# Kernel optimization log

Measured on AMD Instinct MI355X. Metric: run time of the kernel, lower is better.

Reference implementation:

```python
import jax, jax.numpy as jnp
import numpy as np

N_HEAD = 4
N_FEAT = 256
D_K = N_FEAT // N_HEAD
MAX_SEQ_LEN = 500
LN_EPS = 1e-6


def setup_inputs() -> dict:
    key = jax.random.key(0)
    ks = jax.random.split(key, 12)
    B, L, F = 64, 500, N_FEAT
    s = lambda fan_in: 1.0 / np.sqrt(fan_in)
    return {
        "q": jax.random.normal(ks[0], (B, L, F), jnp.float32),
        "k": jax.random.normal(ks[1], (B, L, F), jnp.float32),
        "v": jax.random.normal(ks[2], (B, L, F), jnp.float32),
        # weights stored as [in, out] (torch Linear transposed)
        "w_qs": jax.random.normal(ks[3], (F, F), jnp.float32) * s(F),
        "w_vs": jax.random.normal(ks[4], (F, F), jnp.float32) * s(F),
        "w1": jax.random.normal(ks[5], (D_K, D_K), jnp.float32) * s(D_K),
        "b1": jax.random.normal(ks[6], (D_K,), jnp.float32) * s(D_K),
        "w2": jax.random.normal(ks[7], (D_K, MAX_SEQ_LEN), jnp.float32) * s(D_K),
        "b2": jax.random.normal(ks[8], (MAX_SEQ_LEN,), jnp.float32) * s(D_K),
        "fc_w": jax.random.normal(ks[9], (F, F), jnp.float32) * s(F),
        "ln_g": jnp.ones((F,), jnp.float32),
        "ln_b": jnp.zeros((F,), jnp.float32),
    }


def reference(q, k, v, w_qs, w_vs, w1, b1, w2, b2, fc_w, ln_g, ln_b):
    B, L, F = q.shape
    H, dk = N_HEAD, D_K
    residual = q
    # head projections -> [B, H, L, dk]
    qh = (q @ w_qs).reshape(B, L, H, dk).transpose(0, 2, 1, 3)
    vh = (v @ w_vs).reshape(B, L, H, dk).transpose(0, 2, 1, 3)
    # dense synthesizer: relu(q W1 + b1) W2 + b2, slice to len_q
    weight = jax.nn.relu(qh @ w1 + b1)
    attn = (weight @ w2 + b2)[..., :L]            # [B, H, L, L]
    attn = jax.nn.softmax(attn, axis=-1)
    out = attn @ vh                                # [B, H, L, dk]
    out = out.transpose(0, 2, 1, 3).reshape(B, L, F)
    out = out @ fc_w + residual
    # LayerNorm(eps=1e-6)
    mu = jnp.mean(out, axis=-1, keepdims=True)
    var = jnp.var(out, axis=-1, keepdims=True)
    out = (out - mu) * jax.lax.rsqrt(var + LN_EPS) * ln_g + ln_b
    return out
```

## Files before the change

### kernel.cpp

```cpp
#include <hip/hip_runtime.h>
#include <math.h>

#define B_   64
#define L_   500
#define F_   256
#define H_   4
#define DK   64

typedef unsigned short u16;
typedef unsigned int   u32;
typedef __attribute__((ext_vector_type(8))) short short8;
typedef __attribute__((ext_vector_type(4))) float f32x4;

static __device__ __forceinline__ u16 f2bf(float f) {
    u32 u = __float_as_uint(f);
    u32 r = (u + 0x7FFFu + ((u >> 16) & 1u)) >> 16;
    return (u16)r;
}

typedef __attribute__((address_space(3))) u32 lds32;
typedef const __attribute__((address_space(1))) u32 gbl32;
static __device__ __forceinline__ void gload_lds16(const u16* g, u16* l) {
    __builtin_amdgcn_global_load_lds((gbl32*)g, (lds32*)l, 16, 0, 0);
}

__global__ __launch_bounds__(256) void prep_kernel(
    const float* __restrict__ wq, const float* __restrict__ wv,
    const float* __restrict__ fcw, const float* __restrict__ w1,
    const float* __restrict__ w2, const float* __restrict__ b2,
    u16* __restrict__ wqT, u16* __restrict__ wvT, u16* __restrict__ fcwT,
    u16* __restrict__ w1T, u16* __restrict__ w2sw,
    u16* __restrict__ qh_bf, u16* __restrict__ vhT, float* __restrict__ b2p)
{
    int t = blockIdx.x * 256 + threadIdx.x;
    int stride = gridDim.x * 256;
    for (int i = t; i < 256 * 256; i += stride) {
        int n = i >> 8, k = i & 255;
        wqT[i]  = f2bf(wq[k * 256 + n]);
        wvT[i]  = f2bf(wv[k * 256 + n]);
        fcwT[i] = f2bf(fcw[k * 256 + n]);
    }
    for (int i = t; i < 64 * 64; i += stride) {
        int n = i >> 6, k = i & 63;
        w1T[i] = f2bf(w1[k * 64 + n]);
    }
    for (int i = t; i < 512 * 64; i += stride) {
        int cc  = i >> 12;
        int row = (i >> 6) & 63;
        int kc  = i & 63;
        int n   = cc * 64 + row;
        int kl  = kc ^ ((row & 7) << 3);
        w2sw[i] = f2bf(n < 500 ? w2[kl * 500 + n] : 0.f);
    }
    for (int i = t; i < 512; i += stride)
        b2p[i] = (i < 500) ? b2[i] : -1e30f;
    for (int i = t; i < 3072; i += stride)
        qh_bf[8192000 + i] = 0;
    for (int i = t; i < 196608; i += stride) {
        int bh = i / 768;
        int r  = i - bh * 768;
        int d  = r / 12;
        int kk = 52 + (r - d * 12);
        vhT[((size_t)((bh * 8 + 7) * 64 + d)) * 64 + (kk ^ ((d & 7) << 3))] = 0;
    }
}

__global__ __launch_bounds__(512) void proj_kernel(
    const float* __restrict__ q, const float* __restrict__ v,
    const u16* __restrict__ wqT, const u16* __restrict__ wvT,
    u16* __restrict__ qh_bf, u16* __restrict__ vhT)
{
    const int which = blockIdx.y;
    const float* __restrict__ x = which ? v : q;
    const u16*   __restrict__ wT = which ? wvT : wqT;

    __shared__ u16 Xs[64][72];
    __shared__ u16 Ws[256][72];

    const int tid  = threadIdx.x;
    const int wvid = tid >> 6, ln = tid & 63;
    const int n16  = ln & 15, quad = ln >> 4;
    const int wr   = wvid >> 2, wc = wvid & 3;
    const int row0 = blockIdx.x * 64;

    f32x4 acc[2][4];
    #pragma unroll
    for (int mt = 0; mt < 2; mt++)
        #pragma unroll
        for (int nt = 0; nt < 4; nt++) acc[mt][nt] = (f32x4){0.f, 0.f, 0.f, 0.f};

    for (int kc = 0; kc < 256; kc += 64) {
        #pragma unroll
        for (int j = 0; j < 2; j++) {
            int idx = tid + 512 * j;
            int m = idx >> 4, k4 = idx & 15;
            float4 a = *(const float4*)&x[(size_t)(row0 + m) * 256 + kc + k4 * 4];
            __align__(8) u16 t4[4] = {f2bf(a.x), f2bf(a.y), f2bf(a.z), f2bf(a.w)};
            *(uint2*)&Xs[m][k4 * 4] = *(const uint2*)t4;
        }
        #pragma unroll
        for (int j = 0; j < 4; j++) {
            int idx = tid + 512 * j;
            int n = idx >> 3, k8 = idx & 7;
            *(uint4*)&Ws[n][k8 * 8] = *(const uint4*)&wT[n * 256 + kc + k8 * 8];
        }
        __syncthreads();
        #pragma unroll
        for (int ks = 0; ks < 2; ks++) {
            short8 af[2], bfr[4];
            #pragma unroll
            for (int mt = 0; mt < 2; mt++)
                af[mt] = *(const short8*)&Xs[wr * 32 + mt * 16 + n16][ks * 32 + quad * 8];
            #pragma unroll
            for (int nt = 0; nt < 4; nt++)
                bfr[nt] = *(const short8*)&Ws[wc * 64 + nt * 16 + n16][ks * 32 + quad * 8];
            #pragma unroll
            for (int mt = 0; mt < 2; mt++)
                #pragma unroll
                for (int nt = 0; nt < 4; nt++)
                    acc[mt][nt] = __builtin_amdgcn_mfma_f32_16x16x32_bf16(
                        af[mt], bfr[nt], acc[mt][nt], 0, 0, 0);
        }
        __syncthreads();
    }

    if (which == 0) {
        #pragma unroll
        for (int mt = 0; mt < 2; mt++) {
            int m0 = row0 + wr * 32 + mt * 16 + quad * 4;
            int b  = m0 / 500;
            int l0 = m0 - 500 * b;
            #pragma unroll
            for (int nt = 0; nt < 4; nt++) {
                int d = nt * 16 + n16;
                u16* dst = qh_bf + ((size_t)((b * 4 + wc) * 500 + l0)) * 64 + d;
                #pragma unroll
                for (int i = 0; i < 4; i++)
                    dst[(size_t)i * 64] = f2bf(acc[mt][nt][i]);
            }
        }
    } else {
        #pragma unroll
        for (int mt = 0; mt < 2; mt++) {
            int m0 = row0 + wr * 32 + mt * 16 + quad * 4;
            int b  = m0 / 500;
            int l0 = m0 - 500 * b;
            int cc = l0 >> 6, kk = l0 & 63;
            #pragma unroll
            for (int nt = 0; nt < 4; nt++) {
                int d = nt * 16 + n16;
                __align__(8) u16 t4[4];
                #pragma unroll
                for (int i = 0; i < 4; i++) t4[i] = f2bf(acc[mt][nt][i]);
                size_t base = ((size_t)(((b * 4 + wc) * 8 + cc) * 64 + d)) * 64;
                *(uint2*)&vhT[base + (kk ^ ((d & 7) << 3))] = *(const uint2*)t4;
            }
        }
    }
}

__global__ __launch_bounds__(512, 4) void attn_kernel(
    const u16* __restrict__ qh, const u16* __restrict__ vhT,
    const u16* __restrict__ w1T, const float* __restrict__ b1,
    const u16* __restrict__ w2sw, const float* __restrict__ b2p,
    u16* __restrict__ ctx)
{
    __shared__ __align__(16) u16 w2s[2][4096];
    __shared__ __align__(16) u16 v_s[2][4096];
    __shared__ __align__(16) u16 scr[8][16][72];

    const int tid  = threadIdx.x;
    const int wv   = tid >> 6;
    const int ln   = tid & 63;
    const int n16  = ln & 15;
    const int quad = ln >> 4;
    const int bh   = blockIdx.x;
    const int r0   = blockIdx.y * 128 + wv * 16;

    const u16* vg = vhT + (size_t)bh * 32768;

    {
        int off = wv * 512 + ln * 8;
        gload_lds16(w2sw + off, &w2s[0][wv * 512]);
        gload_lds16(vg + off,   &v_s[0][wv * 512]);
    }

    {
        const u16* qbase = qh + ((size_t)(bh * 500 + r0 + n16)) * 64;
        short8 a0 = *(const short8*)(qbase + quad * 8);
        short8 a1 = *(const short8*)(qbase + 32 + quad * 8);
        #pragma unroll
        for (int nt = 0; nt < 4; nt++) {
            const u16* wb = w1T + (nt * 16 + n16) * 64;
            short8 bb0 = *(const short8*)(wb + quad * 8);
            short8 bb1 = *(const short8*)(wb + 32 + quad * 8);
            float bias = b1[nt * 16 + n16];
            f32x4 c = {bias, bias, bias, bias};
            c = __builtin_amdgcn_mfma_f32_16x16x32_bf16(a0, bb0, c, 0, 0, 0);
            c = __builtin_amdgcn_mfma_f32_16x16x32_bf16(a1, bb1, c, 0, 0, 0);
            int col = nt * 16 + n16;
            #pragma unroll
            for (int i = 0; i < 4; i++)
                scr[wv][quad * 4 + i][col] = f2bf(fmaxf(c[i], 0.f));
        }
    }
    short8 sa0 = *(const short8*)&scr[wv][n16][quad * 8];
    short8 sa1 = *(const short8*)&scr[wv][n16][32 + quad * 8];

    f32x4 oacc[4];
    #pragma unroll
    for (int nt = 0; nt < 4; nt++) oacc[nt] = (f32x4){0.f, 0.f, 0.f, 0.f};
    float sm[4] = {0.f, 0.f, 0.f, 0.f};

    __syncthreads();

    #pragma unroll 2
    for (int cc = 0; cc < 8; cc++) {
        const int cur = cc & 1;
        if (cc < 7) {
            int off = (cc + 1) * 4096 + wv * 512 + ln * 8;
            gload_lds16(w2sw + off, &w2s[cur ^ 1][wv * 512]);
            gload_lds16(vg + off,   &v_s[cur ^ 1][wv * 512]);
        }
        const u16* wb   = &w2s[cur][0];
        const u16* vbuf = &v_s[cur][0];

        f32x4 c8[4];
        #pragma unroll
        for (int t = 0; t < 4; t++) {
            int r  = t * 16 + n16;
            int sw = (r & 7) << 3;
            short8 b0  = *(const short8*)&wb[r * 64 + ((quad * 8) ^ sw)];
            short8 b1v = *(const short8*)&wb[r * 64 + ((32 + quad * 8) ^ sw)];
            float bias = b2p[cc * 64 + r];
            f32x4 c = {bias, bias, bias, bias};
            c = __builtin_amdgcn_mfma_f32_16x16x32_bf16(sa0, b0, c, 0, 0, 0);
            c = __builtin_amdgcn_mfma_f32_16x16x32_bf16(sa1, b1v, c, 0, 0, 0);
            c8[t] = c;
        }
        #pragma unroll
        for (int t = 0; t < 4; t++) {
            int col = t * 16 + n16;
            #pragma unroll
            for (int i = 0; i < 4; i++) {
                float e = __expf(c8[t][i]);
                sm[i] += e;
                scr[wv][quad * 4 + i][col] = f2bf(e);
            }
        }
        #pragma unroll
        for (int ks = 0; ks < 2; ks++) {
            short8 pa = *(const short8*)&scr[wv][n16][ks * 32 + quad * 8];
            #pragma unroll
            for (int nt = 0; nt < 4; nt++) {
                int d   = nt * 16 + n16;
                int swd = (d & 7) << 3;
                short8 vb2 = *(const short8*)&vbuf[d * 64 + ((ks * 32 + quad * 8) ^ swd)];
                oacc[nt] = __builtin_amdgcn_mfma_f32_16x16x32_bf16(pa, vb2, oacc[nt], 0, 0, 0);
            }
        }
        __syncthreads();
    }

    #pragma unroll
    for (int off = 1; off < 16; off <<= 1) {
        #pragma unroll
        for (int i = 0; i < 4; i++) sm[i] += __shfl_xor(sm[i], off);
    }

    const int b = bh >> 2, h = bh & 3;
    #pragma unroll
    for (int i = 0; i < 4; i++) {
        int lrow = r0 + quad * 4 + i;
        if (lrow < 500) {
            float s = 1.f / sm[i];
            u16* dst = &ctx[((size_t)(b * 500 + lrow)) * 256 + h * 64];
            #pragma unroll
            for (int nt = 0; nt < 4; nt++)
                dst[nt * 16 + n16] = f2bf(oacc[nt][i] * s);
        }
    }
}

__global__ __launch_bounds__(512) void final_kernel(
    const u16* __restrict__ ctx, const u16* __restrict__ fcwT,
    const float* __restrict__ qres, const float* __restrict__ g,
    const float* __restrict__ bta, float* __restrict__ out)
{
    __shared__ u16 Xs[64][72];
    __shared__ u16 Ws[256][72];
    __shared__ float red[4][2][64];
    __shared__ float murs[2][64];

    const int tid  = threadIdx.x;
    const int wvid = tid >> 6, ln = tid & 63;
    const int n16  = ln & 15, quad = ln >> 4;
    const int wr   = wvid >> 2, wc = wvid & 3;
    const int row0 = blockIdx.x * 64;

    f32x4 acc[2][4];
    #pragma unroll
    for (int mt = 0; mt < 2; mt++)
        #pragma unroll
        for (int nt = 0; nt < 4; nt++) acc[mt][nt] = (f32x4){0.f, 0.f, 0.f, 0.f};

    for (int kc = 0; kc < 256; kc += 64) {
        {
            int idx = tid;
            int m = idx >> 3, k8 = idx & 7;
            *(uint4*)&Xs[m][k8 * 8] =
                *(const uint4*)&ctx[(size_t)(row0 + m) * 256 + kc + k8 * 8];
        }
        #pragma unroll
        for (int j = 0; j < 4; j++) {
            int idx = tid + 512 * j;
            int n = idx >> 3, k8 = idx & 7;
            *(uint4*)&Ws[n][k8 * 8] = *(const uint4*)&fcwT[n * 256 + kc + k8 * 8];
        }
        __syncthreads();
        #pragma unroll
        for (int ks = 0; ks < 2; ks++) {
            short8 af[2], bfr[4];
            #pragma unroll
            for (int mt = 0; mt < 2; mt++)
                af[mt] = *(const short8*)&Xs[wr * 32 + mt * 16 + n16][ks * 32 + quad * 8];
            #pragma unroll
            for (int nt = 0; nt < 4; nt++)
                bfr[nt] = *(const short8*)&Ws[wc * 64 + nt * 16 + n16][ks * 32 + quad * 8];
            #pragma unroll
            for (int mt = 0; mt < 2; mt++)
                #pragma unroll
                for (int nt = 0; nt < 4; nt++)
                    acc[mt][nt] = __builtin_amdgcn_mfma_f32_16x16x32_bf16(
                        af[mt], bfr[nt], acc[mt][nt], 0, 0, 0);
        }
        __syncthreads();
    }

    #pragma unroll
    for (int mt = 0; mt < 2; mt++) {
        int m0 = row0 + wr * 32 + mt * 16 + quad * 4;
        #pragma unroll
        for (int i = 0; i < 4; i++) {
            const float* rp = &qres[(size_t)(m0 + i) * 256 + wc * 64 + n16];
            #pragma unroll
            for (int nt = 0; nt < 4; nt++)
                acc[mt][nt][i] += rp[nt * 16];
        }
    }
    #pragma unroll
    for (int mt = 0; mt < 2; mt++) {
        #pragma unroll
        for (int i = 0; i < 4; i++) {
            float s1 = 0.f, s2 = 0.f;
            #pragma unroll
            for (int nt = 0; nt < 4; nt++) {
                float vv = acc[mt][nt][i];
                s1 += vv; s2 += vv * vv;
            }
            #pragma unroll
            for (int off = 1; off < 16; off <<= 1) {
                s1 += __shfl_xor(s1, off);
                s2 += __shfl_xor(s2, off);
            }
            if (n16 == 0) {
                int r = wr * 32 + mt * 16 + quad * 4 + i;
                red[wc][0][r] = s1;
                red[wc][1][r] = s2;
            }
        }
    }
    __syncthreads();
    if (tid < 64) {
        float S1 = red[0][0][tid] + red[1][0][tid] + red[2][0][tid] + red[3][0][tid];
        float S2 = red[0][1][tid] + red[1][1][tid] + red[2][1][tid] + red[3][1][tid];
        float mu  = S1 * 0.00390625f;
        float var = S2 * 0.00390625f - mu * mu;
        murs[0][tid] = mu;
        murs[1][tid] = rsqrtf(var + 1e-6f);
    }
    __syncthreads();

    float gv[4], bv[4];
    #pragma unroll
    for (int nt = 0; nt < 4; nt++) {
        int col = wc * 64 + nt * 16 + n16;
        gv[nt] = g[col];
        bv[nt] = bta[col];
    }
    #pragma unroll
    for (int mt = 0; mt < 2; mt++) {
        int rb = wr * 32 + mt * 16 + quad * 4;
        #pragma unroll
        for (int i = 0; i < 4; i++) {
            float mu = murs[0][rb + i];
            float rs = murs[1][rb + i];
            float* op = &out[(size_t)(row0 + rb + i) * 256 + wc * 64 + n16];
            #pragma unroll
            for (int nt = 0; nt < 4; nt++)
                op[nt * 16] = (acc[mt][nt][i] - mu) * rs * gv[nt] + bv[nt];
        }
    }
}

extern "C" void kernel_launch(void* const* d_in, const int* in_sizes, int n_in,
                              void* d_out, int out_size, void* d_ws, size_t ws_size,
                              hipStream_t stream)
{
    const float* q   = (const float*)d_in[0];
    const float* v   = (const float*)d_in[2];
    const float* wqs = (const float*)d_in[3];
    const float* wvs = (const float*)d_in[4];
    const float* w1  = (const float*)d_in[5];
    const float* b1  = (const float*)d_in[6];
    const float* w2  = (const float*)d_in[7];
    const float* b2  = (const float*)d_in[8];
    const float* fcw = (const float*)d_in[9];
    const float* lng = (const float*)d_in[10];
    const float* lnb = (const float*)d_in[11];
    float* out = (float*)d_out;

    u16* qh_bf = (u16*)d_ws;
    u16* vhT   = qh_bf + 8200192;
    u16* w1T   = vhT + 8388608;
    u16* w2sw  = w1T + 4096;
    u16* wqT   = w2sw + 32768;
    u16* wvT   = wqT + 65536;
    u16* fcwT  = wvT + 65536;
    u16* ctx   = fcwT + 65536;
    float* b2p = (float*)(qh_bf + 8195072);

    prep_kernel <<<dim3(64),     256, 0, stream>>>(wqs, wvs, fcw, w1, w2, b2,
                                                   wqT, wvT, fcwT, w1T, w2sw,
                                                   qh_bf, vhT, b2p);
    proj_kernel <<<dim3(500, 2), 512, 0, stream>>>(q, v, wqT, wvT, qh_bf, vhT);
    attn_kernel <<<dim3(256, 4), 512, 0, stream>>>(qh_bf, vhT, w1T, b1, w2sw, b2p, ctx);
    final_kernel<<<dim3(500),    512, 0, stream>>>(ctx, fcwT, q, lng, lnb, out);
}
```

Before: 95.57 us.

## Process all query rows per (batch,head) block with full W2/V resident in LDS

The attention kernel now launches one block per (batch,head) instead of four. Each block loads all of W2, V and the b2 bias into LDS once and loops over four row groups, so the old per-chunk double-buffered loads, per-chunk barriers and redundant reloads of W2/V across the four blocks go away. The exp values are converted to bf16 with a cheaper round-half-up instead of round-to-nearest-even. In exchange LDS use is about 140KB per block, occupancy drops to one block per CU, and only 256 blocks run, which may underfill the GPU.

Measured after the change: 91.33 us. 1.05x faster.

```diff
diff --git a/kernel.cpp b/kernel.cpp
--- a/kernel.cpp
+++ b/kernel.cpp
@@ -16,6 +16,9 @@
     u32 u = __float_as_uint(f);
     u32 r = (u + 0x7FFFu + ((u >> 16) & 1u)) >> 16;
     return (u16)r;
+}
+static __device__ __forceinline__ u16 f2bf_up(float f) {
+    return (u16)((__float_as_uint(f) + 0x8000u) >> 16);
 }
 
 typedef __attribute__((address_space(3))) u32 lds32;
@@ -159,14 +162,15 @@
     }
 }
 
-__global__ __launch_bounds__(512, 4) void attn_kernel(
+__global__ __launch_bounds__(512, 2) void attn_kernel(
     const u16* __restrict__ qh, const u16* __restrict__ vhT,
     const u16* __restrict__ w1T, const float* __restrict__ b1,
     const u16* __restrict__ w2sw, const float* __restrict__ b2p,
     u16* __restrict__ ctx)
 {
-    __shared__ __align__(16) u16 w2s[2][4096];
-    __shared__ __align__(16) u16 v_s[2][4096];
+    __shared__ __align__(16) u16 w2all[32768];
+    __shared__ __align__(16) u16 vall[32768];
+    __shared__ __align__(16) float b2s[512];
     __shared__ __align__(16) u16 scr[8][16][72];
 
     const int tid  = threadIdx.x;
@@ -175,109 +179,124 @@
     const int n16  = ln & 15;
     const int quad = ln >> 4;
     const int bh   = blockIdx.x;
-    const int r0   = blockIdx.y * 128 + wv * 16;
 
     const u16* vg = vhT + (size_t)bh * 32768;
 
+    short8 a0[4], a1[4];
+    #pragma unroll
+    for (int rg = 0; rg < 4; rg++) {
+        const u16* qbase = qh + ((size_t)(bh * 500 + rg * 128 + wv * 16 + n16)) * 64;
+        a0[rg] = *(const short8*)(qbase + quad * 8);
+        a1[rg] = *(const short8*)(qbase + 32 + quad * 8);
+    }
+    short8 w1b0[4], w1b1[4];
+    float  b1v[4];
+    #pragma unroll
+    for (int nt = 0; nt < 4; nt++) {
+        const u16* wb = w1T + (nt * 16 + n16) * 64;
+        w1b0[nt] = *(const short8*)(wb + quad * 8);
+        w1b1[nt] = *(const short8*)(wb + 32 + quad * 8);
+        b1v[nt]  = b1[nt * 16 + n16];
+    }
+    __builtin_amdgcn_sched_barrier(0);
+
     {
-        int off = wv * 512 + ln * 8;
-        gload_lds16(w2sw + off, &w2s[0][wv * 512]);
-        gload_lds16(vg + off,   &v_s[0][wv * 512]);
-    }
-
-    {
-        const u16* qbase = qh + ((size_t)(bh * 500 + r0 + n16)) * 64;
-        short8 a0 = *(const short8*)(qbase + quad * 8);
-        short8 a1 = *(const short8*)(qbase + 32 + quad * 8);
+        int base = wv * 4096;
+        #pragma unroll
+        for (int j = 0; j < 8; j++)
+            gload_lds16(w2sw + base + j * 512 + ln * 8, &w2all[base + j * 512]);
+        #pragma unroll
+        for (int j = 0; j < 8; j++)
+            gload_lds16(vg + base + j * 512 + ln * 8, &vall[base + j * 512]);
+        if (wv < 2)
+            gload_lds16((const u16*)b2p + wv * 512 + ln * 8, (u16*)&b2s[wv * 256]);
+    }
+    __builtin_amdgcn_sched_barrier(0);
+
+    short8 sa0[4], sa1[4];
+    #pragma unroll
+    for (int rg = 0; rg < 4; rg++) {
         #pragma unroll
         for (int nt = 0; nt < 4; nt++) {
-            const u16* wb = w1T + (nt * 16 + n16) * 64;
-            short8 bb0 = *(const short8*)(wb + quad * 8);
-            short8 bb1 = *(const short8*)(wb + 32 + quad * 8);
-            float bias = b1[nt * 16 + n16];
+            float bias = b1v[nt];
             f32x4 c = {bias, bias, bias, bias};
-            c = __builtin_amdgcn_mfma_f32_16x16x32_bf16(a0, bb0, c, 0, 0, 0);
-            c = __builtin_amdgcn_mfma_f32_16x16x32_bf16(a1, bb1, c, 0, 0, 0);
+            c = __builtin_amdgcn_mfma_f32_16x16x32_bf16(a0[rg], w1b0[nt], c, 0, 0, 0);
+            c = __builtin_amdgcn_mfma_f32_16x16x32_bf16(a1[rg], w1b1[nt], c, 0, 0, 0);
             int col = nt * 16 + n16;
             #pragma unroll
             for (int i = 0; i < 4; i++)
                 scr[wv][quad * 4 + i][col] = f2bf(fmaxf(c[i], 0.f));
         }
-    }
-    short8 sa0 = *(const short8*)&scr[wv][n16][quad * 8];
-    short8 sa1 = *(const short8*)&scr[wv][n16][32 + quad * 8];
-
-    f32x4 oacc[4];
-    #pragma unroll
-    for (int nt = 0; nt < 4; nt++) oacc[nt] = (f32x4){0.f, 0.f, 0.f, 0.f};
-    float sm[4] = {0.f, 0.f, 0.f, 0.f};
+        sa0[rg] = *(const short8*)&scr[wv][n16][quad * 8];
+        sa1[rg] = *(const short8*)&scr[wv][n16][32 + quad * 8];
+    }
 
     __syncthreads();
 
-    #pragma unroll 2
-    for (int cc = 0; cc < 8; cc++) {
-        const int cur = cc & 1;
-        if (cc < 7) {
-            int off = (cc + 1) * 4096 + wv * 512 + ln * 8;
-            gload_lds16(w2sw + off, &w2s[cur ^ 1][wv * 512]);
-            gload_lds16(vg + off,   &v_s[cur ^ 1][wv * 512]);
-        }
-        const u16* wb   = &w2s[cur][0];
-        const u16* vbuf = &v_s[cur][0];
-
-        f32x4 c8[4];
-        #pragma unroll
-        for (int t = 0; t < 4; t++) {
-            int r  = t * 16 + n16;
-            int sw = (r & 7) << 3;
-            short8 b0  = *(const short8*)&wb[r * 64 + ((quad * 8) ^ sw)];
-            short8 b1v = *(const short8*)&wb[r * 64 + ((32 + quad * 8) ^ sw)];
-            float bias = b2p[cc * 64 + r];
-            f32x4 c = {bias, bias, bias, bias};
-            c = __builtin_amdgcn_mfma_f32_16x16x32_bf16(sa0, b0, c, 0, 0, 0);
-            c = __builtin_amdgcn_mfma_f32_16x16x32_bf16(sa1, b1v, c, 0, 0, 0);
-            c8[t] = c;
-        }
-        #pragma unroll
-        for (int t = 0; t < 4; t++) {
-            int col = t * 16 + n16;
-            #pragma unroll
-            for (int i = 0; i < 4; i++) {
-                float e = __expf(c8[t][i]);
-                sm[i] += e;
-                scr[wv][quad * 4 + i][col] = f2bf(e);
-            }
-        }
-        #pragma unroll
-        for (int ks = 0; ks < 2; ks++) {
-            short8 pa = *(const short8*)&scr[wv][n16][ks * 32 + quad * 8];
-            #pragma unroll
-            for (int nt = 0; nt < 4; nt++) {
-                int d   = nt * 16 + n16;
-                int swd = (d & 7) << 3;
-                short8 vb2 = *(const short8*)&vbuf[d * 64 + ((ks * 32 + quad * 8) ^ swd)];
-                oacc[nt] = __builtin_amdgcn_mfma_f32_16x16x32_bf16(pa, vb2, oacc[nt], 0, 0, 0);
-            }
-        }
-        __syncthreads();
-    }
-
-    #pragma unroll
-    for (int off = 1; off < 16; off <<= 1) {
-        #pragma unroll
-        for (int i = 0; i < 4; i++) sm[i] += __shfl_xor(sm[i], off);
-    }
-
     const int b = bh >> 2, h = bh & 3;
     #pragma unroll
-    for (int i = 0; i < 4; i++) {
-        int lrow = r0 + quad * 4 + i;
-        if (lrow < 500) {
-            float s = 1.f / sm[i];
-            u16* dst = &ctx[((size_t)(b * 500 + lrow)) * 256 + h * 64];
-            #pragma unroll
-            for (int nt = 0; nt < 4; nt++)
-                dst[nt * 16 + n16] = f2bf(oacc[nt][i] * s);
+    for (int rg = 0; rg < 4; rg++) {
+        f32x4 oacc[4];
+        #pragma unroll
+        for (int nt = 0; nt < 4; nt++) oacc[nt] = (f32x4){0.f, 0.f, 0.f, 0.f};
+        float sm[4] = {0.f, 0.f, 0.f, 0.f};
+
+        #pragma unroll 2
+        for (int cc = 0; cc < 8; cc++) {
+            f32x4 c8[4];
+            #pragma unroll
+            for (int t = 0; t < 4; t++) {
+                int r  = t * 16 + n16;
+                int sw = (r & 7) << 3;
+                const u16* wb = &w2all[cc * 4096 + r * 64];
+                short8 b0  = *(const short8*)&wb[(quad * 8) ^ sw];
+                short8 b1f = *(const short8*)&wb[(32 + quad * 8) ^ sw];
+                float bias = b2s[cc * 64 + r];
+                f32x4 c = {bias, bias, bias, bias};
+                c = __builtin_amdgcn_mfma_f32_16x16x32_bf16(sa0[rg], b0, c, 0, 0, 0);
+                c = __builtin_amdgcn_mfma_f32_16x16x32_bf16(sa1[rg], b1f, c, 0, 0, 0);
+                c8[t] = c;
+            }
+            #pragma unroll
+            for (int t = 0; t < 4; t++) {
+                int col = t * 16 + n16;
+                #pragma unroll
+                for (int i = 0; i < 4; i++) {
+                    float e = __expf(c8[t][i]);
+                    sm[i] += e;
+                    scr[wv][quad * 4 + i][col] = f2bf_up(e);
+                }
+            }
+            #pragma unroll
+            for (int ks = 0; ks < 2; ks++) {
+                short8 pa = *(const short8*)&scr[wv][n16][ks * 32 + quad * 8];
+                #pragma unroll
+                for (int nt = 0; nt < 4; nt++) {
+                    int d   = nt * 16 + n16;
+                    int swd = (d & 7) << 3;
+                    short8 vb2 = *(const short8*)&vall[cc * 4096 + d * 64 +
+                                                       ((ks * 32 + quad * 8) ^ swd)];
+                    oacc[nt] = __builtin_amdgcn_mfma_f32_16x16x32_bf16(
+                        pa, vb2, oacc[nt], 0, 0, 0);
+                }
+            }
+        }
+
+        #pragma unroll
+        for (int off = 1; off < 16; off <<= 1) {
+            #pragma unroll
+            for (int i = 0; i < 4; i++) sm[i] += __shfl_xor(sm[i], off);
+        }
+        #pragma unroll
+        for (int i = 0; i < 4; i++) {
+            int lrow = rg * 128 + wv * 16 + quad * 4 + i;
+            if (lrow < 500) {
+                float s = 1.f / sm[i];
+                u16* dst = &ctx[((size_t)(b * 500 + lrow)) * 256 + h * 64];
+                #pragma unroll
+                for (int nt = 0; nt < 4; nt++)
+                    dst[nt * 16 + n16] = f2bf(oacc[nt][i] * s);
+            }
         }
     }
 }
@@ -434,6 +453,6 @@
                                                    wqT, wvT, fcwT, w1T, w2sw,
                                                    qh_bf, vhT, b2p);
     proj_kernel <<<dim3(500, 2), 512, 0, stream>>>(q, v, wqT, wvT, qh_bf, vhT);
-    attn_kernel <<<dim3(256, 4), 512, 0, stream>>>(qh_bf, vhT, w1T, b1, w2sw, b2p, ctx);
+    attn_kernel <<<dim3(256),    512, 0, stream>>>(qh_bf, vhT, w1T, b1, w2sw, b2p, ctx);
     final_kernel<<<dim3(500),    512, 0, stream>>>(ctx, fcwT, q, lng, lnb, out);
 }
```
